# Performance work log

Measured on AMD Instinct MI355X. Metric: run time of the kernel, lower is better.

Reference implementation:

```python
import jax, jax.numpy as jnp
import numpy as np

EPS = 1e-6
NUM_HEADS = 8
HEAD_DIM = 64


def _elu_plus_one(x):
    # ELU(x) + 1 : positive feature map used for linear attention
    return jax.nn.elu(x) + 1.0


def setup_inputs() -> dict:
    key = jax.random.key(0)
    ks = jax.random.split(key, 10)
    B, S, D = 1, 4096, 512  # batch, seq_len, hidden_size
    P = NUM_HEADS * HEAD_DIM  # proj_dim == hidden_size here
    scale = 0.05  # keep projections numerically tame
    return {
        "hidden_states": jax.random.normal(ks[0], (B, S, D), jnp.float32),
        "Wq": jax.random.normal(ks[1], (D, P), jnp.float32) * scale,
        "bq": jnp.zeros((P,), jnp.float32),
        "Wk": jax.random.normal(ks[2], (D, P), jnp.float32) * scale,
        "bk": jnp.zeros((P,), jnp.float32),
        "Wv": jax.random.normal(ks[3], (D, P), jnp.float32) * scale,
        "bv": jnp.zeros((P,), jnp.float32),
        "Wo": jax.random.normal(ks[4], (P, D), jnp.float32) * scale,
        # persistent per-head tensor-product memory: M [H, Dh, Dh], z [H, Dh]
        "M_mem": jax.random.uniform(ks[5], (NUM_HEADS, HEAD_DIM, HEAD_DIM), jnp.float32),
        "z_mem": jax.random.uniform(ks[6], (NUM_HEADS, HEAD_DIM), jnp.float32),
    }


def reference(hidden_states, Wq, bq, Wk, bk, Wv, bv, Wo, M_mem, z_mem):
    B, S, D = hidden_states.shape
    H, Dh = NUM_HEADS, HEAD_DIM

    def split_heads(t):
        # [B, S, H*Dh] -> [B, H, S, Dh]
        return t.reshape(B, S, H, Dh).transpose(0, 2, 1, 3)

    q = split_heads(hidden_states @ Wq + bq)
    k = split_heads(hidden_states @ Wk + bk)
    v = split_heads(hidden_states @ Wv + bv)

    sq = _elu_plus_one(q)  # sigma(Q)  [B,H,S,Dh]
    sk = _elu_plus_one(k)  # sigma(K)  [B,H,S,Dh]

    # kv[t] = sigma(k_t) (x) v_t ; causal prefix sums, seeded by persistent memory
    kv = sk[..., :, None] * v[..., None, :]            # [B,H,S,Dh,Dh]
    cumsum_kv = jnp.cumsum(kv, axis=2) + M_mem[None, :, None]  # + M per head
    cumsum_k = jnp.cumsum(sk, axis=2) + z_mem[None, :, None]   # + z per head

    numerator = jnp.einsum('bhsd,bhsde->bhse', sq, cumsum_kv)  # [B,H,S,Dh]
    denominator = jnp.einsum('bhsd,bhsd->bhs', sq, cumsum_k)   # [B,H,S]
    out = numerator / (denominator[..., None] + EPS)

    out = out.transpose(0, 2, 1, 3).reshape(B, S, H * Dh)  # merge heads
    return out @ Wo
```

## Files before the change

### kernel.cpp

```cpp
#include <hip/hip_runtime.h>
#include <hip/hip_bf16.h>
#include <math.h>

#define S_LEN 4096
#define D_HID 512
#define P_DIM 512
#define H_NUM 8
#define DH 64
#define NC 64
#define EPS 1e-6f

typedef __attribute__((ext_vector_type(8))) short short8;
typedef __attribute__((ext_vector_type(4))) float f32x4;
typedef __attribute__((ext_vector_type(4))) unsigned short ushort4v;

static __device__ __forceinline__ float b2f(unsigned short u) {
  return __builtin_bit_cast(float, ((unsigned int)u) << 16);
}
static __device__ __forceinline__ unsigned short f2b(float f) {
  unsigned int u = __builtin_bit_cast(unsigned int, f);
  u = (u + 0x7fff + ((u >> 16) & 1)) >> 16;
  return (unsigned short)u;
}
static __device__ __forceinline__ int swz(int row, int d) {
  return d ^ ((row & 7) << 3);
}

#define GLOAD_LDS16(g, l)                                              \
  __builtin_amdgcn_global_load_lds(                                    \
      (const __attribute__((address_space(1))) unsigned int*)(g),      \
      (__attribute__((address_space(3))) unsigned int*)(l), 16, 0, 0)

__global__ __launch_bounds__(256) void prep_kernel(
    const float* __restrict__ hs, const float* __restrict__ Wq,
    const float* __restrict__ Wk, const float* __restrict__ Wv,
    const float* __restrict__ Wo, unsigned short* __restrict__ hs_bf,
    unsigned short* __restrict__ WT) {
  __shared__ float t[32][33];
  int bid = blockIdx.x, tid = threadIdx.x;
  if (bid < 2048) {
    int idx = bid * 256 + tid;
    float4 v = ((const float4*)hs)[idx];
    ushort4v o = {f2b(v.x), f2b(v.y), f2b(v.z), f2b(v.w)};
    *(ushort4v*)(hs_bf + (size_t)idx * 4) = o;
  } else {
    int b2 = bid - 2048;
    int z = b2 >> 8, r = b2 & 255;
    const float* src = (z == 0) ? Wq : (z == 1) ? Wk : (z == 2) ? Wv : Wo;
    int bx = (r & 15) * 32;
    int by = (r >> 4) * 32;
    int lx = tid & 31, ly = tid >> 5;
#pragma unroll
    for (int i = 0; i < 4; i++)
      t[ly + i * 8][lx] = src[(size_t)(by + ly + i * 8) * 512 + bx + lx];
    __syncthreads();
#pragma unroll
    for (int i = 0; i < 4; i++) {
      int n = bx + ly + i * 8;
      WT[((size_t)z * 512 + n) * 512 + by + lx] = f2b(t[lx][ly + i * 8]);
    }
  }
}

template <int MODE>
__global__ __launch_bounds__(256) void mfma_gemm(
    const unsigned short* __restrict__ A, const unsigned short* __restrict__ BT,
    const float* __restrict__ bq, const float* __restrict__ bk,
    const float* __restrict__ bv, unsigned short* __restrict__ sqz,
    unsigned short* __restrict__ skz, unsigned short* __restrict__ skTz,
    unsigned short* __restrict__ vTz, float* __restrict__ outf) {
  union SU {
    struct {
      unsigned short As[64 * 32];
      unsigned short Bs[128 * 32];
    } st;
    unsigned short epsT[128 * 72];
  };
  __shared__ SU sh;
  int tid = threadIdx.x;
  int w = tid >> 6, lane = tid & 63;
  int bm = blockIdx.x * 64, bn = blockIdx.y * 128;
  f32x4 acc[2][4] = {};

  int ldrow = lane >> 2;
  int ldk = (lane & 3) * 8;
  int wr = w >> 1, wc = w & 1;
  int fr = lane & 15, kg8 = (lane >> 4) * 8, q4 = (lane >> 4) * 4;

  for (int k0 = 0; k0 < 512; k0 += 32) {
    GLOAD_LDS16(A + (size_t)(bm + w * 16 + ldrow) * 512 + k0 + ldk,
                sh.st.As + w * 512);
    GLOAD_LDS16(BT + (size_t)(bn + w * 16 + ldrow) * 512 + k0 + ldk,
                sh.st.Bs + w * 512);
    GLOAD_LDS16(BT + (size_t)(bn + (w + 4) * 16 + ldrow) * 512 + k0 + ldk,
                sh.st.Bs + (w + 4) * 512);
    __syncthreads();

    short8 a[2], b[4];
#pragma unroll
    for (int m = 0; m < 2; m++)
      a[m] = *(const short8*)(sh.st.As + (wr * 32 + m * 16 + fr) * 32 + kg8);
#pragma unroll
    for (int n = 0; n < 4; n++)
      b[n] = *(const short8*)(sh.st.Bs + (wc * 64 + n * 16 + fr) * 32 + kg8);
#pragma unroll
    for (int m = 0; m < 2; m++)
#pragma unroll
      for (int n = 0; n < 4; n++)
        acc[m][n] = __builtin_amdgcn_mfma_f32_16x16x32_bf16(a[m], b[n],
                                                            acc[m][n], 0, 0, 0);
    __syncthreads();
  }

  if (MODE == 0) {
    int region = bn >> 9;
    int hh_base = (bn & 511) >> 6;
#pragma unroll
    for (int m = 0; m < 2; m++) {
      int sl0 = wr * 32 + m * 16 + q4;
#pragma unroll
      for (int n = 0; n < 4; n++) {
        int cl = wc * 64 + n * 16 + fr;
        int col = bn + cl;
        int m512 = col & 511;
        int hh = m512 >> 6, dd = m512 & 63;
        float bias = (region == 0) ? bq[m512]
                     : (region == 1) ? bk[m512] : bv[m512];
#pragma unroll
        for (int j = 0; j < 4; j++) {
          int sl = sl0 + j;
          int s = bm + sl;
          float val = acc[m][n][j] + bias;
          if (region < 2) val = (val > 0.f) ? (val + 1.f) : __expf(val);
          unsigned short bb = f2b(val);
          if (region == 0) {
            sqz[((size_t)hh * S_LEN + s) * 64 + swz(s, dd)] = bb;
          } else if (region == 1) {
            skz[((size_t)hh * S_LEN + s) * 64 + swz(s, dd)] = bb;
            sh.epsT[cl * 72 + (sl ^ ((cl & 7) << 3))] = bb;
          } else {
            sh.epsT[cl * 72 + (sl ^ ((cl & 7) << 3))] = bb;
          }
        }
      }
    }
    __syncthreads();
    if (region >= 1) {
      unsigned short* Tdst = (region == 1) ? skTz : vTz;
#pragma unroll
      for (int i = 0; i < 4; i++) {
        int G = tid + 256 * i;
        int gq = G & 7;
        int cl = G >> 3;
        int hh = hh_base + (cl >> 6), dd = cl & 63;
        short8 v8 = *(const short8*)(sh.epsT + cl * 72 + gq * 8);
        *(short8*)(Tdst + ((size_t)(hh * 64 + dd)) * S_LEN + bm + gq * 8) = v8;
      }
    }
  } else {
#pragma unroll
    for (int m = 0; m < 2; m++) {
      int sl0 = wr * 32 + m * 16 + q4;
#pragma unroll
      for (int n = 0; n < 4; n++) {
        int col = bn + wc * 64 + n * 16 + fr;
#pragma unroll
        for (int j = 0; j < 4; j++)
          outf[(size_t)(bm + sl0 + j) * 512 + col] = acc[m][n][j];
      }
    }
  }
}

__global__ __launch_bounds__(256) void chunk_sum_mfma(
    const unsigned short* __restrict__ vTz, const unsigned short* __restrict__ skTz,
    float* __restrict__ KVt, float* __restrict__ ksum) {
  __shared__ unsigned short vt_lds[64 * 64];
  __shared__ unsigned short skt_lds[64 * 64];
  int h = blockIdx.x / NC, c = blockIdx.x % NC;
  int tid = threadIdx.x, w = tid >> 6, lane = tid & 63;
  int lr = lane >> 3, lc = (lane & 7) * 8;
#pragma unroll
  for (int i = 0; i < 2; i++) {
    int seg = w * 2 + i;
    GLOAD_LDS16(vTz + ((size_t)h * 64 + seg * 8 + lr) * S_LEN + c * 64 + lc,
                vt_lds + seg * 512);
    GLOAD_LDS16(skTz + ((size_t)h * 64 + seg * 8 + lr) * S_LEN + c * 64 + lc,
                skt_lds + seg * 512);
  }
  __syncthreads();

  int fr = lane & 15, kg = (lane >> 4) * 8;
  short8 onesA = {};
  if (fr == 0) {
#pragma unroll
    for (int j = 0; j < 8; j++) onesA[j] = (short)0x3F80;
  }
  f32x4 acc[4] = {};
  f32x4 accK[4] = {};
#pragma unroll
  for (int k0 = 0; k0 < 64; k0 += 32) {
    int e = w * 16 + fr;
    short8 a = *(const short8*)(vt_lds + e * 64 + ((k0 + kg) ^ ((e & 7) << 3)));
    short8 b[4];
#pragma unroll
    for (int nt = 0; nt < 4; nt++) {
      int d = nt * 16 + fr;
      b[nt] = *(const short8*)(skt_lds + d * 64 + ((k0 + kg) ^ ((d & 7) << 3)));
    }
#pragma unroll
    for (int nt = 0; nt < 4; nt++)
      acc[nt] = __builtin_amdgcn_mfma_f32_16x16x32_bf16(a, b[nt], acc[nt], 0, 0, 0);
    if (w == 0) {
#pragma unroll
      for (int nt = 0; nt < 4; nt++)
        accK[nt] =
            __builtin_amdgcn_mfma_f32_16x16x32_bf16(onesA, b[nt], accK[nt], 0, 0, 0);
    }
  }
  int e0 = w * 16 + (lane >> 4) * 4;
  size_t base = (size_t)(h * NC + c) * 4096;
#pragma unroll
  for (int nt = 0; nt < 4; nt++)
#pragma unroll
    for (int j = 0; j < 4; j++)
      KVt[base + (size_t)(e0 + j) * 64 + nt * 16 + fr] = acc[nt][j];
  if (w == 0 && lane < 16) {
#pragma unroll
    for (int nt = 0; nt < 4; nt++)
      ksum[(size_t)(h * NC + c) * 64 + nt * 16 + lane] = accK[nt][0];
  }
}

__global__ __launch_bounds__(256) void prefix_kernel(
    const float* __restrict__ KVt, const float* __restrict__ ksum,
    const float* __restrict__ M_mem, const float* __restrict__ z_mem,
    unsigned short* __restrict__ KVpz, unsigned short* __restrict__ zp_bf) {
  int h = blockIdx.x >> 4, g = blockIdx.x & 15;
  int tid = threadIdx.x;
  int entry = g * 256 + tid, e = entry >> 6, d = entry & 63;
  float pref = M_mem[h * 4096 + d * 64 + e];
  size_t i0 = (size_t)(h * NC) * 4096 + (size_t)e * 64 + d;
  size_t o0 = (size_t)(h * NC) * 4096 + (size_t)e * 64 + swz(e, d);
  for (int c = 0; c < NC; c += 4) {
    float v0 = KVt[i0 + (size_t)c * 4096];
    float v1 = KVt[i0 + (size_t)(c + 1) * 4096];
    float v2 = KVt[i0 + (size_t)(c + 2) * 4096];
    float v3 = KVt[i0 + (size_t)(c + 3) * 4096];
    KVpz[o0 + (size_t)c * 4096] = f2b(pref);
    pref += v0;
    KVpz[o0 + (size_t)(c + 1) * 4096] = f2b(pref);
    pref += v1;
    KVpz[o0 + (size_t)(c + 2) * 4096] = f2b(pref);
    pref += v2;
    KVpz[o0 + (size_t)(c + 3) * 4096] = f2b(pref);
    pref += v3;
  }
  if (g == 0 && tid < 64) {
    float zp = z_mem[h * 64 + tid];
    for (int c = 0; c < NC; c += 4) {
      float u0 = ksum[(size_t)(h * NC + c) * 64 + tid];
      float u1 = ksum[(size_t)(h * NC + c + 1) * 64 + tid];
      float u2 = ksum[(size_t)(h * NC + c + 2) * 64 + tid];
      float u3 = ksum[(size_t)(h * NC + c + 3) * 64 + tid];
      zp_bf[(size_t)(h * NC + c) * 64 + tid] = f2b(zp);
      zp += u0;
      zp_bf[(size_t)(h * NC + c + 1) * 64 + tid] = f2b(zp);
      zp += u1;
      zp_bf[(size_t)(h * NC + c + 2) * 64 + tid] = f2b(zp);
      zp += u2;
      zp_bf[(size_t)(h * NC + c + 3) * 64 + tid] = f2b(zp);
      zp += u3;
    }
  }
}

__global__ __launch_bounds__(256) void attn_mfma(
    const unsigned short* __restrict__ sqz, const unsigned short* __restrict__ skz,
    const unsigned short* __restrict__ vTz, const unsigned short* __restrict__ KVpz,
    const unsigned short* __restrict__ zp_bf, unsigned short* __restrict__ attnb) {
  __shared__ unsigned short sq_lds[4096], sk_lds[4096];
  __shared__ unsigned short btv_lds[80 * 64], btm_lds[80 * 64];
  __shared__ unsigned short shi_lds[4096], slo_lds[4096];
  int h = blockIdx.x / NC, c = blockIdx.x % NC;
  int tid = threadIdx.x, w = tid >> 6, lane = tid & 63;

  {
    const unsigned short* sq_g = sqz + ((size_t)h * S_LEN + c * 64) * 64;
    const unsigned short* sk_g = skz + ((size_t)h * S_LEN + c * 64) * 64;
    const unsigned short* km_g = KVpz + (size_t)(h * NC + c) * 4096;
    int lr = lane >> 3, lc = (lane & 7) * 8;
#pragma unroll
    for (int i = 0; i < 2; i++) {
      int seg = w * 2 + i;
      GLOAD_LDS16(sq_g + seg * 512 + lane * 8, sq_lds + seg * 512);
      GLOAD_LDS16(sk_g + seg * 512 + lane * 8, sk_lds + seg * 512);
      GLOAD_LDS16(km_g + seg * 512 + lane * 8, btm_lds + seg * 512);
      GLOAD_LDS16(vTz + ((size_t)h * 64 + seg * 8 + lr) * S_LEN + c * 64 + lc,
                  btv_lds + seg * 512);
    }
  }
  if (tid < 8) {
    short8 one;
#pragma unroll
    for (int j = 0; j < 8; j++) one[j] = (short)0x3F80;
    *(short8*)(btv_lds + 64 * 64 + tid * 8) = one;
    *(short8*)(btm_lds + 64 * 64 + tid * 8) =
        *(const short8*)(zp_bf + (size_t)(h * NC + c) * 64 + tid * 8);
  }
  __syncthreads();

  int fr = lane & 15, kg8 = (lane >> 4) * 8;
  int ta = w * 16 + fr;
  int sw_a = (ta & 7) << 3;

  f32x4 accS[4] = {};
#pragma unroll
  for (int k0 = 0; k0 < 64; k0 += 32) {
    short8 a = *(const short8*)(sq_lds + ta * 64 + ((k0 + kg8) ^ sw_a));
#pragma unroll
    for (int nt = 0; nt < 4; nt++) {
      int tp = nt * 16 + fr;
      short8 b = *(const short8*)(sk_lds + tp * 64 + ((k0 + kg8) ^ ((tp & 7) << 3)));
      accS[nt] = __builtin_amdgcn_mfma_f32_16x16x32_bf16(a, b, accS[nt], 0, 0, 0);
    }
  }
  int r0 = (lane >> 4) * 4;
#pragma unroll
  for (int nt = 0; nt < 4; nt++) {
    int tp = nt * 16 + fr;
#pragma unroll
    for (int j = 0; j < 4; j++) {
      int t = w * 16 + r0 + j;
      float s = (tp <= t) ? accS[nt][j] : 0.f;
      unsigned short hi = f2b(s);
      unsigned short lo = f2b(s - b2f(hi));
      shi_lds[t * 64 + swz(t, tp)] = hi;
      slo_lds[t * 64 + swz(t, tp)] = lo;
    }
  }
  f32x4 acc2[5] = {};
#pragma unroll
  for (int ks = 0; ks < 6; ks++) {
    const unsigned short* asrc = (ks < 2) ? shi_lds : (ks < 4) ? slo_lds : sq_lds;
    const unsigned short* bsrc = (ks < 4) ? btv_lds : btm_lds;
    int ak = (ks & 1) * 32 + kg8;
    short8 a = *(const short8*)(asrc + ta * 64 + (ak ^ sw_a));
#pragma unroll
    for (int nt = 0; nt < 5; nt++) {
      int n = nt * 16 + fr;
      short8 b = *(const short8*)(bsrc + n * 64 + (ak ^ ((n & 7) << 3)));
      acc2[nt] = __builtin_amdgcn_mfma_f32_16x16x32_bf16(a, b, acc2[nt], 0, 0, 0);
    }
  }
  float inv[4];
#pragma unroll
  for (int j = 0; j < 4; j++) {
    float dj = __shfl(acc2[4][j], (lane & 48), 64);
    inv[j] = 1.f / (dj + EPS);
  }
  int srow = c * 64 + w * 16 + r0;
#pragma unroll
  for (int nt = 0; nt < 4; nt++) {
    int col = h * 64 + nt * 16 + fr;
#pragma unroll
    for (int j = 0; j < 4; j++)
      attnb[(size_t)(srow + j) * 512 + col] = f2b(acc2[nt][j] * inv[j]);
  }
}

extern "C" void kernel_launch(void* const* d_in, const int* in_sizes, int n_in,
                              void* d_out, int out_size, void* d_ws,
                              size_t ws_size, hipStream_t stream) {
  const float* hs = (const float*)d_in[0];
  const float* Wq = (const float*)d_in[1];
  const float* bq = (const float*)d_in[2];
  const float* Wk = (const float*)d_in[3];
  const float* bk = (const float*)d_in[4];
  const float* Wv = (const float*)d_in[5];
  const float* bv = (const float*)d_in[6];
  const float* Wo = (const float*)d_in[7];
  const float* M_mem = (const float*)d_in[8];
  const float* z_mem = (const float*)d_in[9];
  float* out = (float*)d_out;

  unsigned short* hs_bf = (unsigned short*)d_ws;
  unsigned short* WT = hs_bf + (size_t)S_LEN * D_HID;
  unsigned short* sqz = WT + (size_t)4 * 512 * 512;
  unsigned short* skz = sqz + (size_t)H_NUM * S_LEN * DH;
  unsigned short* skTz = skz + (size_t)H_NUM * S_LEN * DH;
  unsigned short* vTz = skTz + (size_t)H_NUM * S_LEN * DH;
  unsigned short* attnb = vTz + (size_t)H_NUM * S_LEN * DH;
  unsigned short* KVpz = attnb + (size_t)S_LEN * P_DIM;
  unsigned short* zp_bf = KVpz + (size_t)H_NUM * NC * DH * DH;
  float* KVt = (float*)(zp_bf + (size_t)H_NUM * NC * DH);
  float* ksum = KVt + (size_t)H_NUM * NC * DH * DH;

  prep_kernel<<<3072, 256, 0, stream>>>(hs, Wq, Wk, Wv, Wo, hs_bf, WT);

  dim3 pg(S_LEN / 64, 1536 / 128);
  mfma_gemm<0><<<pg, 256, 0, stream>>>(hs_bf, WT, bq, bk, bv, sqz, skz, skTz,
                                       vTz, nullptr);

  chunk_sum_mfma<<<H_NUM * NC, 256, 0, stream>>>(vTz, skTz, KVt, ksum);
  prefix_kernel<<<H_NUM * 16, 256, 0, stream>>>(KVt, ksum, M_mem, z_mem, KVpz,
                                                zp_bf);
  attn_mfma<<<H_NUM * NC, 256, 0, stream>>>(sqz, skz, vTz, KVpz, zp_bf, attnb);

  dim3 og(S_LEN / 64, 512 / 128);
  mfma_gemm<1><<<og, 256, 0, stream>>>(attnb, WT + (size_t)3 * 512 * 512,
                                       nullptr, nullptr, nullptr, nullptr,
                                       nullptr, nullptr, nullptr, out);
}
```

Baseline: 126.1 us.

## Fuse QKV projection with chunk sums, parallelize prefix scan, double-buffer GEMMs

The QKV projection is restructured so each block computes the q, k and v tiles for one head and one 64-token chunk. It then computes that chunk's KV outer-product sum and k-sum directly from LDS, which removes the separate chunk_sum kernel and the skT global round trip. The prefix kernel splits the 64-chunk scan into four partial segments per thread group to raise parallelism. Both GEMMs now double-buffer their LDS loads so the next k-tile's global-to-LDS copy overlaps the current MFMAs. The fused projection launches fewer blocks (512) with larger per-block work and 12 accumulators, which may reduce occupancy.

After: 121.1 us. -4.0%, faster.

```diff
diff --git a/kernel.cpp b/kernel.cpp
--- a/kernel.cpp
+++ b/kernel.cpp
@@ -30,6 +30,10 @@
   __builtin_amdgcn_global_load_lds(                                    \
       (const __attribute__((address_space(1))) unsigned int*)(g),      \
       (__attribute__((address_space(3))) unsigned int*)(l), 16, 0, 0)
+
+#define MFMA16(a, b, c) __builtin_amdgcn_mfma_f32_16x16x32_bf16(a, b, c, 0, 0, 0)
+
+#define VMCNT0 asm volatile("s_waitcnt vmcnt(0)" ::: "memory")
 
 __global__ __launch_bounds__(256) void prep_kernel(
     const float* __restrict__ hs, const float* __restrict__ Wq,
@@ -62,215 +66,170 @@
   }
 }
 
-template <int MODE>
-__global__ __launch_bounds__(256) void mfma_gemm(
-    const unsigned short* __restrict__ A, const unsigned short* __restrict__ BT,
-    const float* __restrict__ bq, const float* __restrict__ bk,
-    const float* __restrict__ bv, unsigned short* __restrict__ sqz,
-    unsigned short* __restrict__ skz, unsigned short* __restrict__ skTz,
-    unsigned short* __restrict__ vTz, float* __restrict__ outf) {
-  union SU {
+__global__ __launch_bounds__(256) void proj_kernel(
+    const unsigned short* __restrict__ hs_bf,
+    const unsigned short* __restrict__ WT, const float* __restrict__ bq,
+    const float* __restrict__ bk, const float* __restrict__ bv,
+    unsigned short* __restrict__ sqz, unsigned short* __restrict__ skz,
+    unsigned short* __restrict__ vTz, float* __restrict__ KVt,
+    float* __restrict__ ksum) {
+  union U {
     struct {
-      unsigned short As[64 * 32];
-      unsigned short Bs[128 * 32];
+      unsigned short As[2][64 * 32];
+      unsigned short Bs[2][192 * 32];
     } st;
-    unsigned short epsT[128 * 72];
+    struct {
+      unsigned short skT[64 * 64];
+      unsigned short vT[64 * 64];
+    } cs;
   };
-  __shared__ SU sh;
-  int tid = threadIdx.x;
-  int w = tid >> 6, lane = tid & 63;
-  int bm = blockIdx.x * 64, bn = blockIdx.y * 128;
-  f32x4 acc[2][4] = {};
-
-  int ldrow = lane >> 2;
-  int ldk = (lane & 3) * 8;
-  int wr = w >> 1, wc = w & 1;
+  __shared__ U u;
+  int tid = threadIdx.x, w = tid >> 6, lane = tid & 63;
+  int c = blockIdx.x, h = blockIdx.y;
   int fr = lane & 15, kg8 = (lane >> 4) * 8, q4 = (lane >> 4) * 4;
-
-  for (int k0 = 0; k0 < 512; k0 += 32) {
-    GLOAD_LDS16(A + (size_t)(bm + w * 16 + ldrow) * 512 + k0 + ldk,
-                sh.st.As + w * 512);
-    GLOAD_LDS16(BT + (size_t)(bn + w * 16 + ldrow) * 512 + k0 + ldk,
-                sh.st.Bs + w * 512);
-    GLOAD_LDS16(BT + (size_t)(bn + (w + 4) * 16 + ldrow) * 512 + k0 + ldk,
-                sh.st.Bs + (w + 4) * 512);
-    __syncthreads();
-
-    short8 a[2], b[4];
-#pragma unroll
-    for (int m = 0; m < 2; m++)
-      a[m] = *(const short8*)(sh.st.As + (wr * 32 + m * 16 + fr) * 32 + kg8);
-#pragma unroll
-    for (int n = 0; n < 4; n++)
-      b[n] = *(const short8*)(sh.st.Bs + (wc * 64 + n * 16 + fr) * 32 + kg8);
-#pragma unroll
-    for (int m = 0; m < 2; m++)
-#pragma unroll
-      for (int n = 0; n < 4; n++)
-        acc[m][n] = __builtin_amdgcn_mfma_f32_16x16x32_bf16(a[m], b[n],
-                                                            acc[m][n], 0, 0, 0);
-    __syncthreads();
-  }
-
-  if (MODE == 0) {
-    int region = bn >> 9;
-    int hh_base = (bn & 511) >> 6;
-#pragma unroll
-    for (int m = 0; m < 2; m++) {
-      int sl0 = wr * 32 + m * 16 + q4;
-#pragma unroll
-      for (int n = 0; n < 4; n++) {
-        int cl = wc * 64 + n * 16 + fr;
-        int col = bn + cl;
-        int m512 = col & 511;
-        int hh = m512 >> 6, dd = m512 & 63;
-        float bias = (region == 0) ? bq[m512]
-                     : (region == 1) ? bk[m512] : bv[m512];
-#pragma unroll
-        for (int j = 0; j < 4; j++) {
-          int sl = sl0 + j;
-          int s = bm + sl;
-          float val = acc[m][n][j] + bias;
-          if (region < 2) val = (val > 0.f) ? (val + 1.f) : __expf(val);
-          unsigned short bb = f2b(val);
-          if (region == 0) {
-            sqz[((size_t)hh * S_LEN + s) * 64 + swz(s, dd)] = bb;
-          } else if (region == 1) {
-            skz[((size_t)hh * S_LEN + s) * 64 + swz(s, dd)] = bb;
-            sh.epsT[cl * 72 + (sl ^ ((cl & 7) << 3))] = bb;
-          } else {
-            sh.epsT[cl * 72 + (sl ^ ((cl & 7) << 3))] = bb;
-          }
-        }
+  int ldrow = lane >> 2, ldk = (lane & 3) * 8;
+
+  const unsigned short* Ag =
+      hs_bf + (size_t)(c * 64 + w * 16 + ldrow) * 512 + ldk;
+  const unsigned short* Bg =
+      WT + (size_t)(h * 64 + w * 16 + ldrow) * 512 + ldk;
+
+#define PSTAGE(buf, k0)                                              \
+  do {                                                               \
+    GLOAD_LDS16(Ag + (k0), u.st.As[buf] + w * 512);                  \
+    GLOAD_LDS16(Bg + (k0), u.st.Bs[buf] + w * 512);                  \
+    GLOAD_LDS16(Bg + 262144 + (k0), u.st.Bs[buf] + 2048 + w * 512);  \
+    GLOAD_LDS16(Bg + 524288 + (k0), u.st.Bs[buf] + 4096 + w * 512);  \
+  } while (0)
+
+  f32x4 acc[12] = {};
+  PSTAGE(0, 0);
+  VMCNT0;
+  __builtin_amdgcn_s_barrier();
+  int cur = 0;
+  for (int it = 0; it < 16; it++) {
+    if (it < 15) PSTAGE(cur ^ 1, (it + 1) * 32);
+    short8 a = *(const short8*)(u.st.As[cur] + (w * 16 + fr) * 32 + kg8);
+#pragma unroll
+    for (int nt = 0; nt < 12; nt++) {
+      short8 b = *(const short8*)(u.st.Bs[cur] + (nt * 16 + fr) * 32 + kg8);
+      acc[nt] = MFMA16(a, b, acc[nt]);
+    }
+    VMCNT0;
+    __builtin_amdgcn_s_barrier();
+    cur ^= 1;
+  }
+
+#pragma unroll
+  for (int nt = 0; nt < 12; nt++) {
+    int z = nt >> 2, d = (nt & 3) * 16 + fr;
+    float bias = (z == 0) ? bq[h * 64 + d]
+                          : (z == 1) ? bk[h * 64 + d] : bv[h * 64 + d];
+#pragma unroll
+    for (int j = 0; j < 4; j++) {
+      int t = w * 16 + q4 + j;
+      int s = c * 64 + t;
+      float val = acc[nt][j] + bias;
+      if (z < 2) val = (val > 0.f) ? (val + 1.f) : __expf(val);
+      unsigned short bb = f2b(val);
+      if (z == 0) {
+        sqz[((size_t)h * S_LEN + s) * 64 + swz(s, d)] = bb;
+      } else if (z == 1) {
+        skz[((size_t)h * S_LEN + s) * 64 + swz(s, d)] = bb;
+        u.cs.skT[d * 64 + swz(d, t)] = bb;
+      } else {
+        u.cs.vT[d * 64 + swz(d, t)] = bb;
       }
     }
-    __syncthreads();
-    if (region >= 1) {
-      unsigned short* Tdst = (region == 1) ? skTz : vTz;
-#pragma unroll
-      for (int i = 0; i < 4; i++) {
-        int G = tid + 256 * i;
-        int gq = G & 7;
-        int cl = G >> 3;
-        int hh = hh_base + (cl >> 6), dd = cl & 63;
-        short8 v8 = *(const short8*)(sh.epsT + cl * 72 + gq * 8);
-        *(short8*)(Tdst + ((size_t)(hh * 64 + dd)) * S_LEN + bm + gq * 8) = v8;
+  }
+  __syncthreads();
+
+#pragma unroll
+  for (int i = 0; i < 2; i++) {
+    int G = tid + 256 * i;
+    int e = G >> 3, gq = G & 7;
+    *(short8*)(vTz + ((size_t)(h * 64 + e)) * S_LEN + c * 64 + gq * 8) =
+        *(const short8*)(u.cs.vT + e * 64 + gq * 8);
+  }
+
+  {
+    short8 onesA = {};
+    if (fr == 0) {
+#pragma unroll
+      for (int j = 0; j < 8; j++) onesA[j] = (short)0x3F80;
+    }
+    f32x4 accC[4] = {}, accKk[4] = {};
+#pragma unroll
+    for (int k0 = 0; k0 < 64; k0 += 32) {
+      int e = w * 16 + fr;
+      short8 a2 =
+          *(const short8*)(u.cs.vT + e * 64 + ((k0 + kg8) ^ ((e & 7) << 3)));
+#pragma unroll
+      for (int nt = 0; nt < 4; nt++) {
+        int d = nt * 16 + fr;
+        short8 b2 = *(const short8*)(u.cs.skT + d * 64 +
+                                     ((k0 + kg8) ^ ((d & 7) << 3)));
+        accC[nt] = MFMA16(a2, b2, accC[nt]);
+        if (w == 0) accKk[nt] = MFMA16(onesA, b2, accKk[nt]);
       }
     }
-  } else {
-#pragma unroll
-    for (int m = 0; m < 2; m++) {
-      int sl0 = wr * 32 + m * 16 + q4;
-#pragma unroll
-      for (int n = 0; n < 4; n++) {
-        int col = bn + wc * 64 + n * 16 + fr;
-#pragma unroll
-        for (int j = 0; j < 4; j++)
-          outf[(size_t)(bm + sl0 + j) * 512 + col] = acc[m][n][j];
-      }
-    }
-  }
-}
-
-__global__ __launch_bounds__(256) void chunk_sum_mfma(
-    const unsigned short* __restrict__ vTz, const unsigned short* __restrict__ skTz,
-    float* __restrict__ KVt, float* __restrict__ ksum) {
-  __shared__ unsigned short vt_lds[64 * 64];
-  __shared__ unsigned short skt_lds[64 * 64];
-  int h = blockIdx.x / NC, c = blockIdx.x % NC;
-  int tid = threadIdx.x, w = tid >> 6, lane = tid & 63;
-  int lr = lane >> 3, lc = (lane & 7) * 8;
-#pragma unroll
-  for (int i = 0; i < 2; i++) {
-    int seg = w * 2 + i;
-    GLOAD_LDS16(vTz + ((size_t)h * 64 + seg * 8 + lr) * S_LEN + c * 64 + lc,
-                vt_lds + seg * 512);
-    GLOAD_LDS16(skTz + ((size_t)h * 64 + seg * 8 + lr) * S_LEN + c * 64 + lc,
-                skt_lds + seg * 512);
-  }
-  __syncthreads();
-
-  int fr = lane & 15, kg = (lane >> 4) * 8;
-  short8 onesA = {};
-  if (fr == 0) {
-#pragma unroll
-    for (int j = 0; j < 8; j++) onesA[j] = (short)0x3F80;
-  }
-  f32x4 acc[4] = {};
-  f32x4 accK[4] = {};
-#pragma unroll
-  for (int k0 = 0; k0 < 64; k0 += 32) {
-    int e = w * 16 + fr;
-    short8 a = *(const short8*)(vt_lds + e * 64 + ((k0 + kg) ^ ((e & 7) << 3)));
-    short8 b[4];
-#pragma unroll
-    for (int nt = 0; nt < 4; nt++) {
-      int d = nt * 16 + fr;
-      b[nt] = *(const short8*)(skt_lds + d * 64 + ((k0 + kg) ^ ((d & 7) << 3)));
-    }
+    size_t base = (size_t)(h * NC + c) * 4096;
+    int e0 = w * 16 + q4;
 #pragma unroll
     for (int nt = 0; nt < 4; nt++)
-      acc[nt] = __builtin_amdgcn_mfma_f32_16x16x32_bf16(a, b[nt], acc[nt], 0, 0, 0);
-    if (w == 0) {
+#pragma unroll
+      for (int j = 0; j < 4; j++)
+        KVt[base + (size_t)(e0 + j) * 64 + nt * 16 + fr] = accC[nt][j];
+    if (w == 0 && lane < 16) {
 #pragma unroll
       for (int nt = 0; nt < 4; nt++)
-        accK[nt] =
-            __builtin_amdgcn_mfma_f32_16x16x32_bf16(onesA, b[nt], accK[nt], 0, 0, 0);
-    }
-  }
-  int e0 = w * 16 + (lane >> 4) * 4;
-  size_t base = (size_t)(h * NC + c) * 4096;
-#pragma unroll
-  for (int nt = 0; nt < 4; nt++)
-#pragma unroll
-    for (int j = 0; j < 4; j++)
-      KVt[base + (size_t)(e0 + j) * 64 + nt * 16 + fr] = acc[nt][j];
-  if (w == 0 && lane < 16) {
-#pragma unroll
-    for (int nt = 0; nt < 4; nt++)
-      ksum[(size_t)(h * NC + c) * 64 + nt * 16 + lane] = accK[nt][0];
-  }
-}
-
-__global__ __launch_bounds__(256) void prefix_kernel(
+        ksum[(size_t)(h * NC + c) * 64 + nt * 16 + lane] = accKk[nt][0];
+    }
+  }
+#undef PSTAGE
+}
+
+__global__ __launch_bounds__(256) void prefix2_kernel(
     const float* __restrict__ KVt, const float* __restrict__ ksum,
     const float* __restrict__ M_mem, const float* __restrict__ z_mem,
     unsigned short* __restrict__ KVpz, unsigned short* __restrict__ zp_bf) {
-  int h = blockIdx.x >> 4, g = blockIdx.x & 15;
+  __shared__ float p[64 * 4];
+  __shared__ float zz[64 * 4];
+  int h = blockIdx.x >> 6, seg = blockIdx.x & 63;
   int tid = threadIdx.x;
-  int entry = g * 256 + tid, e = entry >> 6, d = entry & 63;
-  float pref = M_mem[h * 4096 + d * 64 + e];
-  size_t i0 = (size_t)(h * NC) * 4096 + (size_t)e * 64 + d;
-  size_t o0 = (size_t)(h * NC) * 4096 + (size_t)e * 64 + swz(e, d);
-  for (int c = 0; c < NC; c += 4) {
-    float v0 = KVt[i0 + (size_t)c * 4096];
-    float v1 = KVt[i0 + (size_t)(c + 1) * 4096];
-    float v2 = KVt[i0 + (size_t)(c + 2) * 4096];
-    float v3 = KVt[i0 + (size_t)(c + 3) * 4096];
-    KVpz[o0 + (size_t)c * 4096] = f2b(pref);
-    pref += v0;
-    KVpz[o0 + (size_t)(c + 1) * 4096] = f2b(pref);
-    pref += v1;
-    KVpz[o0 + (size_t)(c + 2) * 4096] = f2b(pref);
-    pref += v2;
-    KVpz[o0 + (size_t)(c + 3) * 4096] = f2b(pref);
-    pref += v3;
-  }
-  if (g == 0 && tid < 64) {
-    float zp = z_mem[h * 64 + tid];
-    for (int c = 0; c < NC; c += 4) {
-      float u0 = ksum[(size_t)(h * NC + c) * 64 + tid];
-      float u1 = ksum[(size_t)(h * NC + c + 1) * 64 + tid];
-      float u2 = ksum[(size_t)(h * NC + c + 2) * 64 + tid];
-      float u3 = ksum[(size_t)(h * NC + c + 3) * 64 + tid];
-      zp_bf[(size_t)(h * NC + c) * 64 + tid] = f2b(zp);
-      zp += u0;
-      zp_bf[(size_t)(h * NC + c + 1) * 64 + tid] = f2b(zp);
-      zp += u1;
-      zp_bf[(size_t)(h * NC + c + 2) * 64 + tid] = f2b(zp);
-      zp += u2;
-      zp_bf[(size_t)(h * NC + c + 3) * 64 + tid] = f2b(zp);
-      zp += u3;
+  int d = tid & 63, q = tid >> 6;
+  size_t ebase = (size_t)h * NC * 4096 + (size_t)seg * 64 + d;
+  float part = 0.f;
+#pragma unroll 4
+  for (int i = 0; i < 16; i++)
+    part += KVt[ebase + (size_t)(q * 16 + i) * 4096];
+  p[d * 4 + q] = part;
+  if (seg == 0) {
+    size_t zb = (size_t)h * NC * 64 + d;
+    float pz = 0.f;
+#pragma unroll 4
+    for (int i = 0; i < 16; i++) pz += ksum[zb + (size_t)(q * 16 + i) * 64];
+    zz[d * 4 + q] = pz;
+  }
+  __syncthreads();
+  float pref = M_mem[h * 4096 + d * 64 + seg];
+  for (int q2 = 0; q2 < q; q2++) pref += p[d * 4 + q2];
+  int sw = swz(seg, d);
+#pragma unroll 4
+  for (int i = 0; i < 16; i++) {
+    int cc = q * 16 + i;
+    KVpz[(size_t)(h * NC + cc) * 4096 + seg * 64 + sw] = f2b(pref);
+    pref += KVt[ebase + (size_t)cc * 4096];
+  }
+  if (seg == 0) {
+    float bz = z_mem[h * 64 + d];
+    for (int q2 = 0; q2 < q; q2++) bz += zz[d * 4 + q2];
+    size_t zb = (size_t)h * NC * 64 + d;
+#pragma unroll 4
+    for (int i = 0; i < 16; i++) {
+      int cc = q * 16 + i;
+      zp_bf[zb + (size_t)cc * 64] = f2b(bz);
+      bz += ksum[zb + (size_t)cc * 64];
     }
   }
 }
@@ -321,8 +280,9 @@
 #pragma unroll
     for (int nt = 0; nt < 4; nt++) {
       int tp = nt * 16 + fr;
-      short8 b = *(const short8*)(sk_lds + tp * 64 + ((k0 + kg8) ^ ((tp & 7) << 3)));
-      accS[nt] = __builtin_amdgcn_mfma_f32_16x16x32_bf16(a, b, accS[nt], 0, 0, 0);
+      short8 b =
+          *(const short8*)(sk_lds + tp * 64 + ((k0 + kg8) ^ ((tp & 7) << 3)));
+      accS[nt] = MFMA16(a, b, accS[nt]);
     }
   }
   int r0 = (lane >> 4) * 4;
@@ -350,7 +310,7 @@
     for (int nt = 0; nt < 5; nt++) {
       int n = nt * 16 + fr;
       short8 b = *(const short8*)(bsrc + n * 64 + (ak ^ ((n & 7) << 3)));
-      acc2[nt] = __builtin_amdgcn_mfma_f32_16x16x32_bf16(a, b, acc2[nt], 0, 0, 0);
+      acc2[nt] = MFMA16(a, b, acc2[nt]);
     }
   }
   float inv[4];
@@ -367,6 +327,64 @@
     for (int j = 0; j < 4; j++)
       attnb[(size_t)(srow + j) * 512 + col] = f2b(acc2[nt][j] * inv[j]);
   }
+}
+
+__global__ __launch_bounds__(256) void gemm_out(
+    const unsigned short* __restrict__ A, const unsigned short* __restrict__ BT,
+    float* __restrict__ outf) {
+  __shared__ unsigned short As[2][64 * 32];
+  __shared__ unsigned short Bs[2][128 * 32];
+  int tid = threadIdx.x, w = tid >> 6, lane = tid & 63;
+  int bm = blockIdx.x * 64, bn = blockIdx.y * 128;
+  f32x4 acc[2][4] = {};
+  int ldrow = lane >> 2, ldk = (lane & 3) * 8;
+  int wr = w >> 1, wc = w & 1;
+  int fr = lane & 15, kg8 = (lane >> 4) * 8, q4 = (lane >> 4) * 4;
+  const unsigned short* Ag = A + (size_t)(bm + w * 16 + ldrow) * 512 + ldk;
+  const unsigned short* Bg0 = BT + (size_t)(bn + w * 16 + ldrow) * 512 + ldk;
+  const unsigned short* Bg1 =
+      BT + (size_t)(bn + (w + 4) * 16 + ldrow) * 512 + ldk;
+
+#define OSTAGE(buf, k0)                              \
+  do {                                               \
+    GLOAD_LDS16(Ag + (k0), As[buf] + w * 512);       \
+    GLOAD_LDS16(Bg0 + (k0), Bs[buf] + w * 512);      \
+    GLOAD_LDS16(Bg1 + (k0), Bs[buf] + (w + 4) * 512); \
+  } while (0)
+
+  OSTAGE(0, 0);
+  VMCNT0;
+  __builtin_amdgcn_s_barrier();
+  int cur = 0;
+  for (int it = 0; it < 16; it++) {
+    if (it < 15) OSTAGE(cur ^ 1, (it + 1) * 32);
+    short8 a[2], b[4];
+#pragma unroll
+    for (int m = 0; m < 2; m++)
+      a[m] = *(const short8*)(As[cur] + (wr * 32 + m * 16 + fr) * 32 + kg8);
+#pragma unroll
+    for (int n = 0; n < 4; n++)
+      b[n] = *(const short8*)(Bs[cur] + (wc * 64 + n * 16 + fr) * 32 + kg8);
+#pragma unroll
+    for (int m = 0; m < 2; m++)
+#pragma unroll
+      for (int n = 0; n < 4; n++) acc[m][n] = MFMA16(a[m], b[n], acc[m][n]);
+    VMCNT0;
+    __builtin_amdgcn_s_barrier();
+    cur ^= 1;
+  }
+#pragma unroll
+  for (int m = 0; m < 2; m++) {
+    int sl0 = wr * 32 + m * 16 + q4;
+#pragma unroll
+    for (int n = 0; n < 4; n++) {
+      int col = bn + wc * 64 + n * 16 + fr;
+#pragma unroll
+      for (int j = 0; j < 4; j++)
+        outf[(size_t)(bm + sl0 + j) * 512 + col] = acc[m][n][j];
+    }
+  }
+#undef OSTAGE
 }
 
 extern "C" void kernel_launch(void* const* d_in, const int* in_sizes, int n_in,
@@ -388,8 +406,7 @@
   unsigned short* WT = hs_bf + (size_t)S_LEN * D_HID;
   unsigned short* sqz = WT + (size_t)4 * 512 * 512;
   unsigned short* skz = sqz + (size_t)H_NUM * S_LEN * DH;
-  unsigned short* skTz = skz + (size_t)H_NUM * S_LEN * DH;
-  unsigned short* vTz = skTz + (size_t)H_NUM * S_LEN * DH;
+  unsigned short* vTz = skz + (size_t)H_NUM * S_LEN * DH;
   unsigned short* attnb = vTz + (size_t)H_NUM * S_LEN * DH;
   unsigned short* KVpz = attnb + (size_t)S_LEN * P_DIM;
   unsigned short* zp_bf = KVpz + (size_t)H_NUM * NC * DH * DH;
@@ -398,17 +415,13 @@
 
   prep_kernel<<<3072, 256, 0, stream>>>(hs, Wq, Wk, Wv, Wo, hs_bf, WT);
 
-  dim3 pg(S_LEN / 64, 1536 / 128);
-  mfma_gemm<0><<<pg, 256, 0, stream>>>(hs_bf, WT, bq, bk, bv, sqz, skz, skTz,
-                                       vTz, nullptr);
-
-  chunk_sum_mfma<<<H_NUM * NC, 256, 0, stream>>>(vTz, skTz, KVt, ksum);
-  prefix_kernel<<<H_NUM * 16, 256, 0, stream>>>(KVt, ksum, M_mem, z_mem, KVpz,
-                                                zp_bf);
-  attn_mfma<<<H_NUM * NC, 256, 0, stream>>>(sqz, skz, vTz, KVpz, zp_bf, attnb);
-
-  dim3 og(S_LEN / 64, 512 / 128);
-  mfma_gemm<1><<<og, 256, 0, stream>>>(attnb, WT + (size_t)3 * 512 * 512,
-                                       nullptr, nullptr, nullptr, nullptr,
-                                       nullptr, nullptr, nullptr, out);
-}
+  proj_kernel<<<dim3(NC, H_NUM), 256, 0, stream>>>(hs_bf, WT, bq, bk, bv, sqz,
+                                                   skz, vTz, KVt, ksum);
+
+  prefix2_kernel<<<512, 256, 0, stream>>>(KVt, ksum, M_mem, z_mem, KVpz, zp_bf);
+
+  attn_mfma<<<512, 256, 0, stream>>>(sqz, skz, vTz, KVpz, zp_bf, attnb);
+
+  gemm_out<<<dim3(S_LEN / 64, 512 / 128), 256, 0, stream>>>(
+      attnb, WT + (size_t)3 * 512 * 512, out);
+}
```
